# Optimization experiments

Measured on AMD Instinct MI355X. Metric: run time of the kernel, lower is better.

The kernel has to match this reference:

```python
import jax, jax.numpy as jnp
import numpy as np
from jax import lax


def _compute_Bp(lam):
    # Bʹ[k, j] = 1 / prod_{i != j} (1 - λ_i / λ_j), via log-sum for stability.
    k, n = lam.shape
    ratios = lam[:, :, None] / lam[:, None, :]           # [k, n, n], entry (i, j) = λ_i / λ_j
    eye = jnp.eye(n, dtype=bool)[None]                    # zero out diagonal (log(1-0)=0)
    ratios = jnp.where(eye, jnp.zeros((), ratios.dtype), ratios)
    lnBp = -jnp.sum(jnp.log(1.0 - ratios), axis=1)        # [k, n]
    return jnp.exp(lnBp)


def _linear_recurrence(a, b):
    # s_t = a_t * s_{t-1} + b_t (elementwise, diagonal), parallel associative scan over time.
    def combine(c1, c2):
        a1, b1 = c1
        a2, b2 = c2
        return a1 * a2, b1 * a2 + b2
    return lax.associative_scan(combine, (a, b), axis=0)[1]


def _ldstack_forward(x, R, theta, lnC_r, lnC_i, D, Do):
    b, T, d = x.shape
    k, half_n = theta.shape
    n = 2 * half_n
    m = D.shape[1]

    # average=True path: project d -> k, go time-major, lift to complex
    xp = jnp.einsum('btd,dk->btk', x, R)
    xc = jnp.transpose(xp, (1, 0, 2)).astype(jnp.complex64)      # [T, b, k]

    # unitary_constitute: λ = exp(i * [θ, -θ]) on the unit circle
    lam = jnp.exp(jnp.concatenate([theta, -theta], axis=1) * 1j)  # [k, n] complex64
    Cp = jnp.exp(lnC_r + 1j * lnC_i)                              # [k, n, m] complex64

    Bp = _compute_Bp(lam)                                         # [k, n]
    Bx = xc[..., None] * Bp                                       # [T, b, k, n]
    al = jnp.broadcast_to(lam, (T, b, k, n))                      # α is None for Δ=1

    # standard=True: shift coefficients one step (state lags input)
    zeros = jnp.zeros((1, b, k, n), dtype=jnp.complex64)
    al = jnp.concatenate([zeros, al[:-1]], axis=0)
    Bx = jnp.concatenate([zeros, Bx[:-1]], axis=0)

    s = _linear_recurrence(al, Bx)                                # [T, b, k, n]

    Cs = jnp.einsum('tbkn,knm->tbkm', s, Cp)                      # readout
    Dx = xc[..., None] * D.astype(jnp.complex64)[None, None]      # [T, b, k, m]
    y = Cs + Dx + Do.astype(jnp.complex64)                        # [T, b, k, m]

    y = jnp.mean(y, axis=2)                                       # average over k
    y = jnp.real(y)                                               # [T, b, m]
    return jnp.transpose(y, (1, 0, 2))                            # [b, T, m]


def setup_inputs() -> dict:
    b, T, d = 8, 2048, 128
    k, n, m = 32, 32, 128
    key = jax.random.key(0)
    ks = jax.random.split(key, 7)
    x = jax.random.normal(ks[0], (b, T, d), dtype=jnp.float32)
    R = jax.random.normal(ks[1], (d, k), dtype=jnp.float32)
    theta = jax.random.uniform(ks[2], (k, n // 2), dtype=jnp.float32,
                               minval=-np.pi, maxval=np.pi)
    lnC_r = 1e-4 * jax.random.normal(ks[3], (k, n, m), dtype=jnp.float32)
    lnC_i = 1e-4 * jax.random.normal(ks[4], (k, n, m), dtype=jnp.float32)
    D = jax.random.uniform(ks[5], (k, m), dtype=jnp.float32, minval=-1e-3, maxval=1e-3)
    Do = jax.random.uniform(ks[6], (m,), dtype=jnp.float32, minval=-1e-7, maxval=1e-7)
    return {"x": x, "R": R, "theta": theta, "lnC_r": lnC_r, "lnC_i": lnC_i,
            "D": D, "Do": Do}


def reference(x, R, theta, lnC_r, lnC_i, D, Do):
    return _ldstack_forward(x, R, theta, lnC_r, lnC_i, D, Do)
```

## Files before the change

### kernel.cpp

```cpp
#include <hip/hip_runtime.h>
#include <hip/hip_bf16.h>
#include <math.h>

#define K_  32
#define HN  16
#define N_  32
#define M_  128
#define B_  8
#define T_  2048
#define D_  128
#define BT  (B_*T_)
#define KA  1056
#define CHK 32
#define CL  64
#define NSER (B_*K_*HN)
#define NSC  (NSER*CHK)

typedef short short8 __attribute__((ext_vector_type(8)));
typedef float floatx4 __attribute__((ext_vector_type(4)));
typedef unsigned short ushort_t;
typedef unsigned int uint_t;

__device__ __forceinline__ ushort_t f2bf(float f) {
    __hip_bfloat16 h = __float2bfloat16(f);
    return *reinterpret_cast<ushort_t*>(&h);
}
__device__ __forceinline__ uint_t pack_bf2(float re, float im) {
    return ((uint_t)f2bf(im) << 16) | (uint_t)f2bf(re);
}

__global__ void k_lambp(const float* __restrict__ theta, float* __restrict__ ws) {
    int tid = threadIdx.x;
    int k = tid >> 4, j = tid & 15;
    float angj = theta[k * HN + j];
    float pr = 1.f, pi = 0.f;
    for (int i = 0; i < N_; ++i) {
        if (i == j) continue;
        float angi = (i < HN) ? theta[k * HN + i] : -theta[k * HN + i - HN];
        float d = angi - angj;
        float tr = 1.f - cosf(d);
        float ti = -sinf(d);
        float nr = pr * tr - pi * ti;
        float ni = pr * ti + pi * tr;
        pr = nr; pi = ni;
    }
    float den = pr * pr + pi * pi;
    ws[tid]        = cosf(angj);
    ws[512 + tid]  = sinf(angj);
    ws[1024 + tid] = pr / den;
    ws[1536 + tid] = -pi / den;
}

__global__ void k_weights(const float* __restrict__ lnC_r,
                          const float* __restrict__ lnC_i,
                          const float* __restrict__ D,
                          ushort_t* __restrict__ Wt) {
    int t = blockIdx.x * blockDim.x + threadIdx.x;
    const float inv = 1.f / 32.f;
    if (t < K_ * HN * M_) {
        int m = t & 127, j = (t >> 7) & 15, k = t >> 11;
        int i0 = (k * N_ + j) * M_ + m;
        int i1 = (k * N_ + j + HN) * M_ + m;
        float r0 = expf(lnC_r[i0]), c0 = cosf(lnC_i[i0]), s0 = sinf(lnC_i[i0]);
        float r1 = expf(lnC_r[i1]), c1 = cosf(lnC_i[i1]), s1 = sinf(lnC_i[i1]);
        float wr = (r0 * c0 + r1 * c1) * inv;
        float wi = (r1 * s1 - r0 * s0) * inv;
        *(uint_t*)(Wt + (size_t)m * KA + k * 32 + 2 * j) = pack_bf2(wr, wi);
    } else if (t < K_ * HN * M_ + K_ * M_) {
        int u = t - K_ * HN * M_;
        int m = u & 127, k = u >> 7;
        Wt[(size_t)m * KA + 1024 + k] = f2bf(D[k * M_ + m] * inv);
    }
}

__global__ __launch_bounds__(256) void k_xp(const float* __restrict__ x,
                                            const float* __restrict__ R,
                                            float* __restrict__ xpT,
                                            ushort_t* __restrict__ A2) {
    int kk = threadIdx.x & 31;
    int r8 = threadIdx.x >> 5;
    int row = blockIdx.x * 8 + r8;
    const float* xr = x + (size_t)row * D_;
    float acc = 0.f;
    #pragma unroll 8
    for (int i = 0; i < D_; ++i) acc += xr[i] * R[i * K_ + kk];
    int b = row >> 11, tt = row & 2047;
    A2[(size_t)(tt * 8 + b) * KA + 1024 + kk] = f2bf(acc);
    size_t base = (size_t)(b * K_ + kk) * T_;
    if (tt < T_ - 1) xpT[base + tt + 1] = acc;
    if (tt == 0)     xpT[base] = 0.f;
}

__global__ __launch_bounds__(256) void k_scan_ends(const float* __restrict__ xpT,
                                                   const float* __restrict__ ws,
                                                   float* __restrict__ E) {
    int gid = blockIdx.x * 256 + threadIdx.x;
    int j = gid & 15, c = (gid >> 4) & 31, k = (gid >> 9) & 31, b = gid >> 14;
    int col = k * 16 + j;
    float lr = ws[col], li = ws[512 + col], br = ws[1024 + col], bi = ws[1536 + col];
    float sr = 0.f, si = 0.f;
    const float4* xv4 = (const float4*)(xpT + (size_t)(b * K_ + k) * T_ + c * CL);
    for (int u = 0; u < CL / 4; ++u) {
        float4 xv = xv4[u];
        #pragma unroll
        for (int v = 0; v < 4; ++v) {
            float x1 = (v == 0) ? xv.x : (v == 1) ? xv.y : (v == 2) ? xv.z : xv.w;
            float nr = br * x1 + lr * sr - li * si;
            float ni = bi * x1 + lr * si + li * sr;
            sr = nr; si = ni;
        }
    }
    size_t eidx = ((size_t)(b * 32 + k) * 32 + c) * 16 + j;
    E[eidx] = sr;
    E[NSC + eidx] = si;
}

__global__ void k_carries(const float* __restrict__ ws,
                          const float* __restrict__ E,
                          float* __restrict__ S) {
    int tid = blockIdx.x * blockDim.x + threadIdx.x;
    int j = tid & 15, k = (tid >> 4) & 31, b = tid >> 9;
    int col = k * 16 + j;
    float lr = ws[col], li = ws[512 + col];
    float pr = lr, pi = li;
    #pragma unroll
    for (int q = 0; q < 6; ++q) {
        float nr = pr * pr - pi * pi;
        float ni = 2.f * pr * pi;
        pr = nr; pi = ni;
    }
    float sr = 0.f, si = 0.f;
    size_t base = (size_t)(b * 32 + k) * 32 * 16 + j;
    for (int c = 0; c < CHK; ++c) {
        size_t idx = base + (size_t)c * 16;
        S[idx] = sr;
        S[NSC + idx] = si;
        float er = E[idx], ei = E[NSC + idx];
        float nr = pr * sr - pi * si + er;
        float ni = pr * si + pi * sr + ei;
        sr = nr; si = ni;
    }
}

__global__ __launch_bounds__(256) void k_scan_write(const float* __restrict__ xpT,
                                                    const float* __restrict__ ws,
                                                    const float* __restrict__ S,
                                                    uint_t* __restrict__ A2u) {
    int gid = blockIdx.x * 256 + threadIdx.x;
    int j = gid & 15, c = (gid >> 4) & 31, k = (gid >> 9) & 31, b = gid >> 14;
    int col = k * 16 + j;
    float lr = ws[col], li = ws[512 + col], br = ws[1024 + col], bi = ws[1536 + col];
    size_t sidx = ((size_t)(b * 32 + k) * 32 + c) * 16 + j;
    float sr = S[sidx], si = S[NSC + sidx];
    int t0 = c * CL;
    const float4* xv4 = (const float4*)(xpT + (size_t)(b * K_ + k) * T_ + t0);
    uint_t* Ab = A2u + (size_t)(t0 * 8 + b) * (KA / 2) + col;
    for (int u = 0; u < CL / 4; ++u) {
        float4 xv = xv4[u];
        #pragma unroll
        for (int v = 0; v < 4; ++v) {
            float x1 = (v == 0) ? xv.x : (v == 1) ? xv.y : (v == 2) ? xv.z : xv.w;
            float nr = br * x1 + lr * sr - li * si;
            float ni = bi * x1 + lr * si + li * sr;
            sr = nr; si = ni;
            Ab[0] = pack_bf2(sr, si);
            Ab += 8 * (KA / 2);
        }
    }
}

__global__ __launch_bounds__(256, 4) void k_gemm(const ushort_t* __restrict__ A2,
                                                 const ushort_t* __restrict__ Wt,
                                                 const float* __restrict__ Do,
                                                 float* __restrict__ out) {
    int tid = threadIdx.x;
    int wave = tid >> 6;
    int lane = tid & 63;
    int l16 = lane & 15;
    int quad = lane >> 4;
    int row0 = blockIdx.x * 16;

    const ushort_t* Ap = A2 + (size_t)(row0 + l16) * KA + quad * 8;
    const ushort_t* W0 = Wt + (size_t)(wave * 32 + l16) * KA + quad * 8;
    const ushort_t* W1 = W0 + (size_t)16 * KA;

    floatx4 acc0 = (floatx4){0.f, 0.f, 0.f, 0.f};
    floatx4 acc1 = (floatx4){0.f, 0.f, 0.f, 0.f};

    for (int g = 0; g < 11; ++g) {
        int k0 = g * 96;
        short8 a0  = *(const short8*)(Ap + k0);
        short8 a1  = *(const short8*)(Ap + k0 + 32);
        short8 a2  = *(const short8*)(Ap + k0 + 64);
        short8 b00 = *(const short8*)(W0 + k0);
        short8 b01 = *(const short8*)(W1 + k0);
        short8 b10 = *(const short8*)(W0 + k0 + 32);
        short8 b11 = *(const short8*)(W1 + k0 + 32);
        short8 b20 = *(const short8*)(W0 + k0 + 64);
        short8 b21 = *(const short8*)(W1 + k0 + 64);
        acc0 = __builtin_amdgcn_mfma_f32_16x16x32_bf16(a0, b00, acc0, 0, 0, 0);
        acc1 = __builtin_amdgcn_mfma_f32_16x16x32_bf16(a0, b01, acc1, 0, 0, 0);
        acc0 = __builtin_amdgcn_mfma_f32_16x16x32_bf16(a1, b10, acc0, 0, 0, 0);
        acc1 = __builtin_amdgcn_mfma_f32_16x16x32_bf16(a1, b11, acc1, 0, 0, 0);
        acc0 = __builtin_amdgcn_mfma_f32_16x16x32_bf16(a2, b20, acc0, 0, 0, 0);
        acc1 = __builtin_amdgcn_mfma_f32_16x16x32_bf16(a2, b21, acc1, 0, 0, 0);
    }

    #pragma unroll
    for (int n = 0; n < 2; ++n) {
        int col = wave * 32 + n * 16 + l16;
        float dov = Do[col];
        floatx4 a = n ? acc1 : acc0;
        #pragma unroll
        for (int q = 0; q < 4; ++q) {
            int r = row0 + quad * 4 + q;
            int b = r & 7, t = r >> 3;
            out[(size_t)(b * T_ + t) * M_ + col] = a[q] + dov;
        }
    }
}

extern "C" void kernel_launch(void* const* d_in, const int* in_sizes, int n_in,
                              void* d_out, int out_size, void* d_ws, size_t ws_size,
                              hipStream_t stream) {
    const float* x     = (const float*)d_in[0];
    const float* R     = (const float*)d_in[1];
    const float* theta = (const float*)d_in[2];
    const float* lnC_r = (const float*)d_in[3];
    const float* lnC_i = (const float*)d_in[4];
    const float* D     = (const float*)d_in[5];
    const float* Do    = (const float*)d_in[6];
    float* out = (float*)d_out;

    float* wsf   = (float*)d_ws;
    float* lambp = wsf;
    ushort_t* Wt = (ushort_t*)(wsf + 2048);
    ushort_t* A2 = (ushort_t*)(wsf + 2048 + 67584);
    float* xpT   = wsf + 2048 + 67584 + 8650752;
    float* E     = xpT + (size_t)BT * K_;
    float* S     = E + 2 * (size_t)NSC;

    k_lambp<<<1, 512, 0, stream>>>(theta, lambp);
    k_weights<<<272, 256, 0, stream>>>(lnC_r, lnC_i, D, Wt);
    k_xp<<<BT / 8, 256, 0, stream>>>(x, R, xpT, A2);
    k_scan_ends<<<NSC / 256, 256, 0, stream>>>(xpT, lambp, E);
    k_carries<<<16, 256, 0, stream>>>(lambp, E, S);
    k_scan_write<<<NSC / 256, 256, 0, stream>>>(xpT, lambp, S, (uint_t*)A2);
    k_gemm<<<BT / 16, 256, 0, stream>>>(A2, Wt, Do, out);
}
```

Measured before the change: 144.7 us.

## Fuse setup kernels into one launch, tile x projection via LDS, widen GEMM tiles

Merges the lambda/B', weight-packing and x-projection kernels into a single block-partitioned launch, removing two launches and their serialization gaps. The x projection now stages 32 rows of x in shared memory and computes 4 rows per thread, so each R load is reused across those rows. The GEMM is retiled so each block covers 32 rows and each wave computes a 16x64 output tile with 4 accumulators, reusing each A fragment across more MFMAs. This roughly halves the block count and raises register use, which lowers occupancy.

```diff
diff --git a/kernel.cpp b/kernel.cpp
--- a/kernel.cpp
+++ b/kernel.cpp
@@ -29,66 +29,85 @@
     return ((uint_t)f2bf(im) << 16) | (uint_t)f2bf(re);
 }
 
-__global__ void k_lambp(const float* __restrict__ theta, float* __restrict__ ws) {
-    int tid = threadIdx.x;
-    int k = tid >> 4, j = tid & 15;
-    float angj = theta[k * HN + j];
-    float pr = 1.f, pi = 0.f;
-    for (int i = 0; i < N_; ++i) {
-        if (i == j) continue;
-        float angi = (i < HN) ? theta[k * HN + i] : -theta[k * HN + i - HN];
-        float d = angi - angj;
-        float tr = 1.f - cosf(d);
-        float ti = -sinf(d);
-        float nr = pr * tr - pi * ti;
-        float ni = pr * ti + pi * tr;
-        pr = nr; pi = ni;
-    }
-    float den = pr * pr + pi * pi;
-    ws[tid]        = cosf(angj);
-    ws[512 + tid]  = sinf(angj);
-    ws[1024 + tid] = pr / den;
-    ws[1536 + tid] = -pi / den;
-}
-
-__global__ void k_weights(const float* __restrict__ lnC_r,
-                          const float* __restrict__ lnC_i,
-                          const float* __restrict__ D,
-                          ushort_t* __restrict__ Wt) {
-    int t = blockIdx.x * blockDim.x + threadIdx.x;
-    const float inv = 1.f / 32.f;
-    if (t < K_ * HN * M_) {
-        int m = t & 127, j = (t >> 7) & 15, k = t >> 11;
-        int i0 = (k * N_ + j) * M_ + m;
-        int i1 = (k * N_ + j + HN) * M_ + m;
-        float r0 = expf(lnC_r[i0]), c0 = cosf(lnC_i[i0]), s0 = sinf(lnC_i[i0]);
-        float r1 = expf(lnC_r[i1]), c1 = cosf(lnC_i[i1]), s1 = sinf(lnC_i[i1]);
-        float wr = (r0 * c0 + r1 * c1) * inv;
-        float wi = (r1 * s1 - r0 * s0) * inv;
-        *(uint_t*)(Wt + (size_t)m * KA + k * 32 + 2 * j) = pack_bf2(wr, wi);
-    } else if (t < K_ * HN * M_ + K_ * M_) {
-        int u = t - K_ * HN * M_;
-        int m = u & 127, k = u >> 7;
-        Wt[(size_t)m * KA + 1024 + k] = f2bf(D[k * M_ + m] * inv);
-    }
-}
-
-__global__ __launch_bounds__(256) void k_xp(const float* __restrict__ x,
-                                            const float* __restrict__ R,
-                                            float* __restrict__ xpT,
-                                            ushort_t* __restrict__ A2) {
-    int kk = threadIdx.x & 31;
-    int r8 = threadIdx.x >> 5;
-    int row = blockIdx.x * 8 + r8;
-    const float* xr = x + (size_t)row * D_;
-    float acc = 0.f;
-    #pragma unroll 8
-    for (int i = 0; i < D_; ++i) acc += xr[i] * R[i * K_ + kk];
-    int b = row >> 11, tt = row & 2047;
-    A2[(size_t)(tt * 8 + b) * KA + 1024 + kk] = f2bf(acc);
-    size_t base = (size_t)(b * K_ + kk) * T_;
-    if (tt < T_ - 1) xpT[base + tt + 1] = acc;
-    if (tt == 0)     xpT[base] = 0.f;
+__global__ __launch_bounds__(256) void k_pre(const float* __restrict__ theta,
+                                             const float* __restrict__ lnC_r,
+                                             const float* __restrict__ lnC_i,
+                                             const float* __restrict__ D,
+                                             const float* __restrict__ x,
+                                             const float* __restrict__ R,
+                                             float* __restrict__ ws,
+                                             ushort_t* __restrict__ Wt,
+                                             float* __restrict__ xpT,
+                                             ushort_t* __restrict__ A2) {
+    __shared__ float xls[32 * 128];
+    int bid = blockIdx.x, tid = threadIdx.x;
+    if (bid == 0) {
+        #pragma unroll
+        for (int rep = 0; rep < 2; ++rep) {
+            int t2 = rep * 256 + tid;
+            int k = t2 >> 4, j = t2 & 15;
+            float angj = theta[k * HN + j];
+            float pr = 1.f, pi = 0.f;
+            for (int i = 0; i < N_; ++i) {
+                if (i == j) continue;
+                float angi = (i < HN) ? theta[k * HN + i] : -theta[k * HN + i - HN];
+                float d = angi - angj;
+                float tr = 1.f - cosf(d);
+                float ti = -sinf(d);
+                float nr = pr * tr - pi * ti;
+                float ni = pr * ti + pi * tr;
+                pr = nr; pi = ni;
+            }
+            float den = pr * pr + pi * pi;
+            ws[t2]        = cosf(angj);
+            ws[512 + t2]  = sinf(angj);
+            ws[1024 + t2] = pr / den;
+            ws[1536 + t2] = -pi / den;
+        }
+    } else if (bid <= 272) {
+        int t = (bid - 1) * 256 + tid;
+        const float inv = 1.f / 32.f;
+        if (t < K_ * HN * M_) {
+            int m = t & 127, j = (t >> 7) & 15, k = t >> 11;
+            int i0 = (k * N_ + j) * M_ + m;
+            int i1 = (k * N_ + j + HN) * M_ + m;
+            float r0 = expf(lnC_r[i0]), c0 = cosf(lnC_i[i0]), s0 = sinf(lnC_i[i0]);
+            float r1 = expf(lnC_r[i1]), c1 = cosf(lnC_i[i1]), s1 = sinf(lnC_i[i1]);
+            float wr = (r0 * c0 + r1 * c1) * inv;
+            float wi = (r1 * s1 - r0 * s0) * inv;
+            *(uint_t*)(Wt + (size_t)m * KA + k * 32 + 2 * j) = pack_bf2(wr, wi);
+        } else if (t < K_ * HN * M_ + K_ * M_) {
+            int u = t - K_ * HN * M_;
+            int m = u & 127, k = u >> 7;
+            Wt[(size_t)m * KA + 1024 + k] = f2bf(D[k * M_ + m] * inv);
+        }
+    } else {
+        int xb = bid - 273;
+        int b = xb >> 6;
+        int tbase = (xb & 63) * 32;
+        const float4* xsrc = (const float4*)(x + ((size_t)b * T_ + tbase) * D_);
+        float4* xd = (float4*)xls;
+        #pragma unroll
+        for (int e = 0; e < 4; ++e) xd[tid + 256 * e] = xsrc[tid + 256 * e];
+        __syncthreads();
+        int kk = tid & 31, rg = tid >> 5;
+        float accv[4] = {0.f, 0.f, 0.f, 0.f};
+        #pragma unroll 4
+        for (int i = 0; i < D_; ++i) {
+            float rv = R[i * K_ + kk];
+            #pragma unroll
+            for (int rr = 0; rr < 4; ++rr)
+                accv[rr] += xls[(rg + 8 * rr) * D_ + i] * rv;
+        }
+        #pragma unroll
+        for (int rr = 0; rr < 4; ++rr) {
+            int tt = tbase + rg + 8 * rr;
+            A2[(size_t)(tt * 8 + b) * KA + 1024 + kk] = f2bf(accv[rr]);
+            size_t base = (size_t)(b * K_ + kk) * T_;
+            if (tt < T_ - 1) xpT[base + tt + 1] = accv[rr];
+            if (tt == 0)     xpT[base] = 0.f;
+        }
+    }
 }
 
 __global__ __launch_bounds__(256) void k_scan_ends(const float* __restrict__ xpT,
@@ -169,53 +188,58 @@
     }
 }
 
-__global__ __launch_bounds__(256, 4) void k_gemm(const ushort_t* __restrict__ A2,
+__global__ __launch_bounds__(256, 2) void k_gemm(const ushort_t* __restrict__ A2,
                                                  const ushort_t* __restrict__ Wt,
                                                  const float* __restrict__ Do,
                                                  float* __restrict__ out) {
     int tid = threadIdx.x;
     int wave = tid >> 6;
+    int rh = wave & 1;
+    int chh = wave >> 1;
     int lane = tid & 63;
     int l16 = lane & 15;
     int quad = lane >> 4;
-    int row0 = blockIdx.x * 16;
+    int row0 = blockIdx.x * 32 + rh * 16;
 
     const ushort_t* Ap = A2 + (size_t)(row0 + l16) * KA + quad * 8;
-    const ushort_t* W0 = Wt + (size_t)(wave * 32 + l16) * KA + quad * 8;
-    const ushort_t* W1 = W0 + (size_t)16 * KA;
-
-    floatx4 acc0 = (floatx4){0.f, 0.f, 0.f, 0.f};
-    floatx4 acc1 = (floatx4){0.f, 0.f, 0.f, 0.f};
+    const ushort_t* Wp = Wt + (size_t)(chh * 64 + l16) * KA + quad * 8;
+
+    floatx4 acc[4];
+    #pragma unroll
+    for (int n = 0; n < 4; ++n) acc[n] = (floatx4){0.f, 0.f, 0.f, 0.f};
 
     for (int g = 0; g < 11; ++g) {
         int k0 = g * 96;
-        short8 a0  = *(const short8*)(Ap + k0);
-        short8 a1  = *(const short8*)(Ap + k0 + 32);
-        short8 a2  = *(const short8*)(Ap + k0 + 64);
-        short8 b00 = *(const short8*)(W0 + k0);
-        short8 b01 = *(const short8*)(W1 + k0);
-        short8 b10 = *(const short8*)(W0 + k0 + 32);
-        short8 b11 = *(const short8*)(W1 + k0 + 32);
-        short8 b20 = *(const short8*)(W0 + k0 + 64);
-        short8 b21 = *(const short8*)(W1 + k0 + 64);
-        acc0 = __builtin_amdgcn_mfma_f32_16x16x32_bf16(a0, b00, acc0, 0, 0, 0);
-        acc1 = __builtin_amdgcn_mfma_f32_16x16x32_bf16(a0, b01, acc1, 0, 0, 0);
-        acc0 = __builtin_amdgcn_mfma_f32_16x16x32_bf16(a1, b10, acc0, 0, 0, 0);
-        acc1 = __builtin_amdgcn_mfma_f32_16x16x32_bf16(a1, b11, acc1, 0, 0, 0);
-        acc0 = __builtin_amdgcn_mfma_f32_16x16x32_bf16(a2, b20, acc0, 0, 0, 0);
-        acc1 = __builtin_amdgcn_mfma_f32_16x16x32_bf16(a2, b21, acc1, 0, 0, 0);
+        short8 a0 = *(const short8*)(Ap + k0);
+        short8 a1 = *(const short8*)(Ap + k0 + 32);
+        short8 a2 = *(const short8*)(Ap + k0 + 64);
+        short8 bv[4][3];
+        #pragma unroll
+        for (int n = 0; n < 4; ++n) {
+            #pragma unroll
+            for (int s = 0; s < 3; ++s)
+                bv[n][s] = *(const short8*)(Wp + (size_t)n * 16 * KA + k0 + s * 32);
+        }
+        #pragma unroll
+        for (int n = 0; n < 4; ++n)
+            acc[n] = __builtin_amdgcn_mfma_f32_16x16x32_bf16(a0, bv[n][0], acc[n], 0, 0, 0);
+        #pragma unroll
+        for (int n = 0; n < 4; ++n)
+            acc[n] = __builtin_amdgcn_mfma_f32_16x16x32_bf16(a1, bv[n][1], acc[n], 0, 0, 0);
+        #pragma unroll
+        for (int n = 0; n < 4; ++n)
+            acc[n] = __builtin_amdgcn_mfma_f32_16x16x32_bf16(a2, bv[n][2], acc[n], 0, 0, 0);
     }
 
     #pragma unroll
-    for (int n = 0; n < 2; ++n) {
-        int col = wave * 32 + n * 16 + l16;
+    for (int n = 0; n < 4; ++n) {
+        int col = chh * 64 + n * 16 + l16;
         float dov = Do[col];
-        floatx4 a = n ? acc1 : acc0;
         #pragma unroll
         for (int q = 0; q < 4; ++q) {
             int r = row0 + quad * 4 + q;
             int b = r & 7, t = r >> 3;
-            out[(size_t)(b * T_ + t) * M_ + col] = a[q] + dov;
+            out[(size_t)(b * T_ + t) * M_ + col] = acc[n][q] + dov;
         }
     }
 }
@@ -240,11 +264,10 @@
     float* E     = xpT + (size_t)BT * K_;
     float* S     = E + 2 * (size_t)NSC;
 
-    k_lambp<<<1, 512, 0, stream>>>(theta, lambp);
-    k_weights<<<272, 256, 0, stream>>>(lnC_r, lnC_i, D, Wt);
-    k_xp<<<BT / 8, 256, 0, stream>>>(x, R, xpT, A2);
+    k_pre<<<785, 256, 0, stream>>>(theta, lnC_r, lnC_i, D, x, R,
+                                   lambp, Wt, xpT, A2);
     k_scan_ends<<<NSC / 256, 256, 0, stream>>>(xpT, lambp, E);
     k_carries<<<16, 256, 0, stream>>>(lambp, E, S);
     k_scan_write<<<NSC / 256, 256, 0, stream>>>(xpT, lambp, S, (uint_t*)A2);
-    k_gemm<<<BT / 16, 256, 0, stream>>>(A2, Wt, Do, out);
-}
+    k_gemm<<<512, 256, 0, stream>>>(A2, Wt, Do, out);
+}
```

New measurement: 132.6 us. 8.4% less time.
